# Optimization experiments

Hardware: AMD Instinct MI355X
Metric: run time of the kernel (lower is better)

## Reference

```python
import jax, jax.numpy as jnp
import numpy as np

N = 4096       # num_nodes (must equal out_features: final div broadcasts [C,N]/[N,1])
IN_F = 1024    # module in_features
OUT_F = 4096   # module out_features == N
F_RAW = 512    # raw node feature dim fed to the in-forward Linear


def setup_inputs() -> dict:
    key = jax.random.key(0)
    ks = jax.random.split(key, 5)
    node_features = jax.random.normal(ks[0], (N, F_RAW), dtype=jnp.float32)
    adjacency_matrix = jax.random.bernoulli(ks[1], 0.004, (N, N)).astype(jnp.float32)
    eye = jnp.eye(N, dtype=jnp.float32)
    A0 = adjacency_matrix * (1.0 - eye)                 # adjacency w/o self loops
    S = (A0 @ A0 + A0) * (1.0 - eye)                    # sibling matrix, zero diag
    mask_hadamard = S[:, None, :]                       # [N,1,N]
    mask_father = adjacency_matrix[:, None, :]          # [N,1,N]
    neighbor_count = jnp.maximum(A0.sum(axis=1, keepdims=True), 1.0)  # [N,1]
    lim = float(1.0 / np.sqrt(F_RAW))
    linear_w = jax.random.uniform(ks[2], (IN_F, F_RAW), minval=-lim, maxval=lim, dtype=jnp.float32)
    linear_b = jax.random.uniform(ks[3], (IN_F,), minval=-lim, maxval=lim, dtype=jnp.float32)
    weight = jax.random.normal(ks[4], (IN_F, OUT_F), dtype=jnp.float32) * float(np.sqrt(2.0 / IN_F))
    return dict(node_features=node_features, adjacency_matrix=adjacency_matrix,
                mask_father=mask_father, neighbor_count=neighbor_count,
                mask_hadamard=mask_hadamard, linear_w=linear_w, linear_b=linear_b,
                weight=weight)


def reference(node_features, adjacency_matrix, mask_father, neighbor_count,
              mask_hadamard, linear_w, linear_b, weight):
    # Linear + projection: wf[n,c]
    x = node_features @ linear_w.T + linear_b           # [N, IN_F]
    wf = x @ weight                                      # [N, C]
    # Original builds masked_hadamard[j,i,c] = wf[i,c]*wf[j,c]*S[i,j] ([N,C,N]),
    # contracts with adjacency over i, masks with adj[k,j], sums over k:
    #   sum_hadamard[c,j] = wf[j,c] * sum_i (sum_k adj[k,j]*adj[k,i]) * S[i,j] * wf[i,c]
    # Fused form avoids the O(N^2 C) intermediates; same math.
    A_out = mask_father[:, 0, :]                         # adj[k,j]  [N,N]
    S = mask_hadamard[:, 0, :]                           # S[i,j]    [N,N]
    G = A_out.T @ adjacency_matrix                       # G[j,i] = sum_k adj[k,j]*adj[k,i]
    P = G * S.T                                          # P[j,i] = G[j,i]*S[i,j]
    sum_hadamard = (wf * (P @ wf)).T                     # [C, N]
    # Final broadcast division exactly as torch: [C,N] / [N,1] (requires C==N)
    return sum_hadamard / jnp.square(neighbor_count)
```

## Files before the change

### kernel.cpp

```cpp
#include <hip/hip_runtime.h>
#include <hip/hip_bf16.h>

typedef __attribute__((ext_vector_type(8))) short s16x8;
typedef __attribute__((ext_vector_type(4))) float f32x4;
typedef __attribute__((ext_vector_type(8))) unsigned short u16x8;

__device__ __forceinline__ float b2f(unsigned short u) {
  union { unsigned int i; float f; } x; x.i = ((unsigned int)u) << 16; return x.f;
}
__device__ __forceinline__ unsigned short f2b(float f) {
  __hip_bfloat16 h = __float2bfloat16(f);
  return *reinterpret_cast<unsigned short*>(&h);
}

#define TILE 128
#define BK 32
#define PCAP 128
#define SCAP 1024

template <int EPI>
__global__ __launch_bounds__(256) void gemm_nt(
    const unsigned short* __restrict__ A,
    const unsigned short* __restrict__ B,
    unsigned short* __restrict__ C,
    int M, int N, int K,
    const float* __restrict__ epi_f)
{
  __shared__ unsigned short As[TILE * BK];
  __shared__ unsigned short Bs[TILE * BK];
  const int tid  = threadIdx.x;
  const int lane = tid & 63;
  const int wave = tid >> 6;
  const int wm = (wave & 1) * 64;
  const int wn = (wave >> 1) * 64;
  const long bm = (long)blockIdx.y * TILE;
  const long bn = (long)blockIdx.x * TILE;

  f32x4 acc[4][4] = {};

  const int kTiles = K / BK;
  for (int kt = 0; kt < kTiles; ++kt) {
    const long kb = (long)kt * BK;
#pragma unroll
    for (int i = 0; i < 2; ++i) {
      const int c0 = (wave * 2 + i) * 64;
      const int c  = c0 + lane;
      const int r  = c >> 2;
      const int cc = ((c & 3) ^ ((c >> 3) & 3)) * 8;
      const unsigned short* ga = A + (bm + r) * (long)K + kb + cc;
      const unsigned short* gb = B + (bn + r) * (long)K + kb + cc;
      __builtin_amdgcn_global_load_lds(
          (const __attribute__((address_space(1))) void*)ga,
          (__attribute__((address_space(3))) void*)(As + c0 * 8), 16, 0, 0);
      __builtin_amdgcn_global_load_lds(
          (const __attribute__((address_space(1))) void*)gb,
          (__attribute__((address_space(3))) void*)(Bs + c0 * 8), 16, 0, 0);
    }
    __syncthreads();

    const int rl = lane & 15;
    const int kqx = ((lane >> 4) ^ ((rl >> 1) & 3)) * 8;
    s16x8 af[4], bfr[4];
#pragma unroll
    for (int mi = 0; mi < 4; ++mi)
      af[mi] = *(const s16x8*)(As + (wm + mi * 16 + rl) * BK + kqx);
#pragma unroll
    for (int ni = 0; ni < 4; ++ni)
      bfr[ni] = *(const s16x8*)(Bs + (wn + ni * 16 + rl) * BK + kqx);
#pragma unroll
    for (int mi = 0; mi < 4; ++mi)
#pragma unroll
      for (int ni = 0; ni < 4; ++ni)
        acc[mi][ni] = __builtin_amdgcn_mfma_f32_16x16x32_bf16(af[mi], bfr[ni], acc[mi][ni], 0, 0, 0);
    __syncthreads();
  }

  const int cl = lane & 15;
  const int rq = (lane >> 4) * 4;
#pragma unroll
  for (int mi = 0; mi < 4; ++mi)
#pragma unroll
    for (int ni = 0; ni < 4; ++ni)
#pragma unroll
      for (int r = 0; r < 4; ++r) {
        const long row = bm + wm + mi * 16 + rq + r;
        const long col = bn + wn + ni * 16 + cl;
        float v = acc[mi][ni][r];
        if (EPI == 1) v += epi_f[col];
        C[row * (long)N + col] = f2b(v);
      }
}

__global__ __launch_bounds__(256) void transpose_f2b(
    const float* __restrict__ in, unsigned short* __restrict__ out, int R, int C)
{
  __shared__ unsigned short tile[64][66];
  const int t = threadIdx.x;
  const long r0 = (long)blockIdx.y * 64;
  const long c0 = (long)blockIdx.x * 64;
#pragma unroll
  for (int i = 0; i < 4; ++i) {
    int v = t + i * 256;
    int r = v >> 4;
    int c = (v & 15) * 4;
    float4 d = *(const float4*)(in + (r0 + r) * (long)C + c0 + c);
    tile[r][c + 0] = f2b(d.x); tile[r][c + 1] = f2b(d.y);
    tile[r][c + 2] = f2b(d.z); tile[r][c + 3] = f2b(d.w);
  }
  __syncthreads();
#pragma unroll
  for (int i = 0; i < 4; ++i) {
    int v = t + i * 256;
    int r = v >> 4;
    int c = (v & 15) * 4;
    ushort4 d;
    d.x = tile[c + 0][r]; d.y = tile[c + 1][r]; d.z = tile[c + 2][r]; d.w = tile[c + 3][r];
    *(ushort4*)(out + (c0 + r) * (long)R + r0 + c) = d;
  }
}

__global__ __launch_bounds__(256) void conv_f2b(
    const float* __restrict__ in, unsigned short* __restrict__ out)
{
  const long e = ((long)blockIdx.x * 256 + threadIdx.x) * 4;
  float4 d = *(const float4*)(in + e);
  ushort4 o;
  o.x = f2b(d.x); o.y = f2b(d.y); o.z = f2b(d.z); o.w = f2b(d.w);
  *(ushort4*)(out + e) = o;
}

__global__ __launch_bounds__(256) void zero_f4(float* __restrict__ p)
{
  const long e = ((long)blockIdx.x * 256 + threadIdx.x) * 4;
  *(float4*)(p + e) = make_float4(0.f, 0.f, 0.f, 0.f);
}

__global__ __launch_bounds__(256) void build_colbits(
    const float* __restrict__ adj, unsigned long long* __restrict__ colb)
{
  const int i = blockIdx.x;
  const int t = threadIdx.x;
  const unsigned long long bit = 1ull << (i & 63);
  const int w = i >> 6;
  const float* r = adj + (long)i * 4096;
#pragma unroll
  for (int q = 0; q < 4; ++q) {
    int c = (t + q * 256) * 4;
    float4 v = *(const float4*)(r + c);
    if (v.x != 0.f) atomicOr(&colb[(long)(c + 0) * 64 + w], bit);
    if (v.y != 0.f) atomicOr(&colb[(long)(c + 1) * 64 + w], bit);
    if (v.z != 0.f) atomicOr(&colb[(long)(c + 2) * 64 + w], bit);
    if (v.w != 0.f) atomicOr(&colb[(long)(c + 3) * 64 + w], bit);
  }
}

__global__ __launch_bounds__(256) void build_P2(
    const float* __restrict__ S, const unsigned long long* __restrict__ colb,
    int* __restrict__ pk, float* __restrict__ pv, int* __restrict__ pcnt)
{
  const int k = blockIdx.x;
  const int t = threadIdx.x;
  const int lane = t & 63;
  __shared__ __align__(16) unsigned long long ck[64];
  __shared__ int jl[SCAP];
  __shared__ float sl[SCAP];
  __shared__ int m;
  if (t == 0) m = 0;
  if (t < 64) ck[t] = colb[(long)k * 64 + t];
  __syncthreads();
  const float* Sr = S + (long)k * 4096;
  const unsigned long long lmask = (1ull << lane) - 1ull;
#pragma unroll
  for (int q = 0; q < 4; ++q) {
    int c = (t + q * 256) * 4;
    float4 v = *(const float4*)(Sr + c);
    float vals[4] = { v.x, v.y, v.z, v.w };
#pragma unroll
    for (int r = 0; r < 4; ++r) {
      float vv = vals[r];
      unsigned long long mask = __ballot(vv != 0.f);
      if (mask) {
        int base;
        if (lane == 0) base = atomicAdd(&m, __popcll(mask));
        base = __shfl(base, 0, 64);
        if (vv != 0.f) {
          int pos = base + __popcll(mask & lmask);
          if (pos < SCAP) { jl[pos] = c + r; sl[pos] = vv; }
        }
      }
    }
  }
  __syncthreads();
  const int mm = min(m, SCAP);
  const int l = t & 7;
  for (int idx = (t >> 3); idx < mm; idx += 32) {
    const int j = jl[idx];
    const ulonglong2* cj = (const ulonglong2*)(colb + (long)j * 64);
    int cnt = 0;
#pragma unroll
    for (int it = 0; it < 4; ++it) {
      ulonglong2 q  = cj[it * 8 + l];
      ulonglong2 cc = *(const ulonglong2*)&ck[it * 16 + l * 2];
      cnt += __popcll(q.x & cc.x) + __popcll(q.y & cc.y);
    }
    cnt += __shfl_down(cnt, 4, 8);
    cnt += __shfl_down(cnt, 2, 8);
    cnt += __shfl_down(cnt, 1, 8);
    if (l == 0 && cnt > 0) {
      int slot = atomicAdd(&pcnt[j], 1);
      if (slot < PCAP) {
        pk[(long)j * PCAP + slot] = k;
        pv[(long)j * PCAP + slot] = (float)cnt * sl[idx];
      }
    }
  }
}

__global__ __launch_bounds__(256) void spmm_fused(
    const int* __restrict__ pk, const float* __restrict__ pv,
    const int* __restrict__ pcnt, const unsigned short* __restrict__ wf,
    const float* __restrict__ nc, float* __restrict__ VO)
{
  __shared__ int   k_l[4][PCAP];
  __shared__ float v_l[4][PCAP];
  __shared__ int   n_s[4];
  const int t = threadIdx.x;
  const int wave = t >> 6;
  const int lane = t & 63;
  const int seg = blockIdx.x;
  const int jb  = blockIdx.y * 4;
  {
    int e0 = t;
    k_l[e0 >> 7][e0 & 127] = pk[(long)(jb + (e0 >> 7)) * PCAP + (e0 & 127)];
    v_l[e0 >> 7][e0 & 127] = pv[(long)(jb + (e0 >> 7)) * PCAP + (e0 & 127)];
    int e1 = t + 256;
    k_l[e1 >> 7][e1 & 127] = pk[(long)(jb + (e1 >> 7)) * PCAP + (e1 & 127)];
    v_l[e1 >> 7][e1 & 127] = pv[(long)(jb + (e1 >> 7)) * PCAP + (e1 & 127)];
    if (t < 4) n_s[t] = min(pcnt[jb + t], PCAP);
  }
  __syncthreads();
  const int j = jb + wave;
  const int n = n_s[wave];
  const int* __restrict__ kk = k_l[wave];
  const float* __restrict__ vv = v_l[wave];
  const int c0 = seg * 512 + lane * 8;

  float acc[8] = {};
  int m = 0;
  for (; m + 8 <= n; m += 8) {
    float vs[8];
    u16x8 d[8];
#pragma unroll
    for (int r = 0; r < 8; ++r) {
      vs[r] = vv[m + r];
      d[r] = *(const u16x8*)(wf + (unsigned)(kk[m + r] * 4096 + c0));
    }
    __builtin_amdgcn_sched_barrier(0);
#pragma unroll
    for (int r = 0; r < 8; ++r)
#pragma unroll
      for (int q = 0; q < 8; ++q)
        acc[q] += vs[r] * b2f(d[r][q]);
  }
  for (; m + 2 <= n; m += 2) {
    const float v0 = vv[m], v1 = vv[m + 1];
    u16x8 a = *(const u16x8*)(wf + (unsigned)(kk[m]     * 4096 + c0));
    u16x8 b = *(const u16x8*)(wf + (unsigned)(kk[m + 1] * 4096 + c0));
#pragma unroll
    for (int q = 0; q < 8; ++q) acc[q] += v0 * b2f(a[q]) + v1 * b2f(b[q]);
  }
  for (; m < n; ++m) {
    const float va = vv[m];
    u16x8 a = *(const u16x8*)(wf + (unsigned)(kk[m] * 4096 + c0));
#pragma unroll
    for (int q = 0; q < 8; ++q) acc[q] += va * b2f(a[q]);
  }
  u16x8 wa = *(const u16x8*)(wf + (unsigned)(j * 4096 + c0));
  float out[8];
#pragma unroll
  for (int q = 0; q < 8; q += 4) {
    float4 nv = *(const float4*)(nc + c0 + q);
    float n4[4] = { nv.x, nv.y, nv.z, nv.w };
#pragma unroll
    for (int r = 0; r < 4; ++r)
      out[q + r] = acc[q + r] * b2f(wa[q + r]) / (n4[r] * n4[r]);
  }
  float* dst = VO + (long)j * 4096 + c0;
  *(float4*)(dst + 0) = make_float4(out[0], out[1], out[2], out[3]);
  *(float4*)(dst + 4) = make_float4(out[4], out[5], out[6], out[7]);
}

__global__ __launch_bounds__(256) void final_transpose(float* __restrict__ D)
{
  const int bx = blockIdx.x, by = blockIdx.y;
  if (by > bx) return;
  const int X = bx * 64, Y = by * 64;
  const bool diag = (bx == by);
  __shared__ float t1[64][65];
  __shared__ float t2[64][65];
  const int t = threadIdx.x;
  const int r0 = t >> 4;
  const int c4 = (t & 15) * 4;
#pragma unroll
  for (int i = 0; i < 4; ++i) {
    int r = r0 + i * 16;
    float4 d = *(const float4*)&D[(long)(Y + r) * 4096 + X + c4];
    t1[r][c4 + 0] = d.x; t1[r][c4 + 1] = d.y; t1[r][c4 + 2] = d.z; t1[r][c4 + 3] = d.w;
    if (!diag) {
      float4 e = *(const float4*)&D[(long)(X + r) * 4096 + Y + c4];
      t2[r][c4 + 0] = e.x; t2[r][c4 + 1] = e.y; t2[r][c4 + 2] = e.z; t2[r][c4 + 3] = e.w;
    }
  }
  __syncthreads();
#pragma unroll
  for (int i = 0; i < 4; ++i) {
    int r = r0 + i * 16;
    float4 o;
    o.x = t1[c4 + 0][r]; o.y = t1[c4 + 1][r]; o.z = t1[c4 + 2][r]; o.w = t1[c4 + 3][r];
    *(float4*)&D[(long)(X + r) * 4096 + Y + c4] = o;
    if (!diag) {
      float4 p;
      p.x = t2[c4 + 0][r]; p.y = t2[c4 + 1][r]; p.z = t2[c4 + 2][r]; p.w = t2[c4 + 3][r];
      *(float4*)&D[(long)(Y + r) * 4096 + X + c4] = p;
    }
  }
}

extern "C" void kernel_launch(void* const* d_in, const int* in_sizes, int n_in,
                              void* d_out, int out_size, void* d_ws, size_t ws_size,
                              hipStream_t stream) {
  const float* nf  = (const float*)d_in[0];
  const float* adj = (const float*)d_in[1];
  const float* nc  = (const float*)d_in[3];
  const float* S   = (const float*)d_in[4];
  const float* lw  = (const float*)d_in[5];
  const float* lb  = (const float*)d_in[6];
  const float* w   = (const float*)d_in[7];

  const int NN = 4096, INF = 1024, FR = 512;
  char* ws = (char*)d_ws;
  unsigned short*      wf      = (unsigned short*)(ws);
  unsigned long long*  colb    = (unsigned long long*)(ws + (32ll << 20));
  int*                 pcnt    = (int*)(ws + (34ll << 20));
  int*                 pk      = (int*)(ws + (35ll << 20));
  float*               pv      = (float*)(ws + (37ll << 20));
  unsigned short*      weightT = (unsigned short*)(ws + (40ll << 20));
  unsigned short*      nfb     = (unsigned short*)(ws + (48ll << 20));
  unsigned short*      lwb     = (unsigned short*)(ws + (52ll << 20));
  unsigned short*      x       = (unsigned short*)(ws + (54ll << 20));
  float*               VO      = (float*)d_out;

  zero_f4<<<516, 256, 0, stream>>>((float*)colb);
  build_colbits<<<NN, 256, 0, stream>>>(adj, colb);
  build_P2<<<NN, 256, 0, stream>>>(S, colb, pk, pv, pcnt);

  transpose_f2b<<<dim3(NN / 64, INF / 64), 256, 0, stream>>>(w, weightT, INF, NN);
  conv_f2b<<<(NN * (long)FR / 4) / 256, 256, 0, stream>>>(nf, nfb);
  conv_f2b<<<(INF * (long)FR / 4) / 256, 256, 0, stream>>>(lw, lwb);
  gemm_nt<1><<<dim3(INF / TILE, NN / TILE), 256, 0, stream>>>(nfb, lwb, x, NN, INF, FR, lb);
  gemm_nt<0><<<dim3(NN / TILE, NN / TILE), 256, 0, stream>>>(x, weightT, wf, NN, NN, INF, nullptr);

  spmm_fused<<<dim3(8, NN / 4), 256, 0, stream>>>(pk, pv, pcnt, wf, nc, VO);

  final_transpose<<<dim3(NN / 64, NN / 64), 256, 0, stream>>>(VO);
}
```

Measured before the change: 393.8 us.

## Double-buffer LDS tiles in bf16 GEMM to overlap global loads with MFMA

Splits the shared-memory A/B tiles into two buffers and issues the async global-to-LDS loads for the next K tile before computing on the current one. A partial vmcnt wait lets the prefetch stay in flight while the MFMAs run, so global load latency is meant to be hidden behind compute. The cost is twice the LDS per block, which may lower occupancy, and the correctness of the hand-written vmcnt count is fragile.

```diff
diff --git a/kernel.cpp b/kernel.cpp
--- a/kernel.cpp
+++ b/kernel.cpp
@@ -26,8 +26,8 @@
     int M, int N, int K,
     const float* __restrict__ epi_f)
 {
-  __shared__ unsigned short As[TILE * BK];
-  __shared__ unsigned short Bs[TILE * BK];
+  __shared__ unsigned short As[2][TILE * BK];
+  __shared__ unsigned short Bs[2][TILE * BK];
   const int tid  = threadIdx.x;
   const int lane = tid & 63;
   const int wave = tid >> 6;
@@ -38,8 +38,7 @@
 
   f32x4 acc[4][4] = {};
 
-  const int kTiles = K / BK;
-  for (int kt = 0; kt < kTiles; ++kt) {
+  auto STAGE = [&](int kt, int b) {
     const long kb = (long)kt * BK;
 #pragma unroll
     for (int i = 0; i < 2; ++i) {
@@ -51,28 +50,46 @@
       const unsigned short* gb = B + (bn + r) * (long)K + kb + cc;
       __builtin_amdgcn_global_load_lds(
           (const __attribute__((address_space(1))) void*)ga,
-          (__attribute__((address_space(3))) void*)(As + c0 * 8), 16, 0, 0);
+          (__attribute__((address_space(3))) void*)(&As[b][c0 * 8]), 16, 0, 0);
       __builtin_amdgcn_global_load_lds(
           (const __attribute__((address_space(1))) void*)gb,
-          (__attribute__((address_space(3))) void*)(Bs + c0 * 8), 16, 0, 0);
-    }
-    __syncthreads();
+          (__attribute__((address_space(3))) void*)(&Bs[b][c0 * 8]), 16, 0, 0);
+    }
+  };
+
+  const int kTiles = K / BK;
+  STAGE(0, 0);
+
+  for (int kt = 0; kt < kTiles; ++kt) {
+    const int cur = kt & 1;
+    if (kt + 1 < kTiles) {
+      STAGE(kt + 1, cur ^ 1);
+      asm volatile("s_waitcnt vmcnt(4)" ::: "memory");
+    } else {
+      asm volatile("s_waitcnt vmcnt(0)" ::: "memory");
+    }
+    __builtin_amdgcn_sched_barrier(0);
+    __builtin_amdgcn_s_barrier();
+    __builtin_amdgcn_sched_barrier(0);
 
     const int rl = lane & 15;
     const int kqx = ((lane >> 4) ^ ((rl >> 1) & 3)) * 8;
     s16x8 af[4], bfr[4];
 #pragma unroll
     for (int mi = 0; mi < 4; ++mi)
-      af[mi] = *(const s16x8*)(As + (wm + mi * 16 + rl) * BK + kqx);
+      af[mi] = *(const s16x8*)(&As[cur][(wm + mi * 16 + rl) * BK + kqx]);
 #pragma unroll
     for (int ni = 0; ni < 4; ++ni)
-      bfr[ni] = *(const s16x8*)(Bs + (wn + ni * 16 + rl) * BK + kqx);
+      bfr[ni] = *(const s16x8*)(&Bs[cur][(wn + ni * 16 + rl) * BK + kqx]);
 #pragma unroll
     for (int mi = 0; mi < 4; ++mi)
 #pragma unroll
       for (int ni = 0; ni < 4; ++ni)
         acc[mi][ni] = __builtin_amdgcn_mfma_f32_16x16x32_bf16(af[mi], bfr[ni], acc[mi][ni], 0, 0, 0);
-    __syncthreads();
+
+    __builtin_amdgcn_sched_barrier(0);
+    __builtin_amdgcn_s_barrier();
+    __builtin_amdgcn_sched_barrier(0);
   }
 
   const int cl = lane & 15;
```

Result: no change. 387.2 us (-1.7%).
